# Kernel tuning notes

Measured on AMD Instinct MI355X. Metric: run time of the kernel, lower is better.

Reference implementation:

```python
import jax, jax.numpy as jnp
import numpy as np

D_IN = 512
N_EXPERTS = 32
HID = 16
BATCH = 262144


def setup_inputs() -> dict:
    key = jax.random.key(0)
    kx, kg, k1, kb1, k2, kb2 = jax.random.split(key, 6)
    x = jax.random.normal(kx, (BATCH, D_IN), dtype=jnp.float32)
    # gating: n_experts independent Linear(d_in, 1, bias=False) -> [E, d_in]
    Wg = jax.random.normal(kg, (N_EXPERTS, D_IN), dtype=jnp.float32) * 0.02
    # experts: Linear(d_in,16) -> GELU -> Linear(16,1)
    W1 = jax.random.normal(k1, (N_EXPERTS, D_IN, HID), dtype=jnp.float32) * 0.02
    b1 = jax.random.normal(kb1, (N_EXPERTS, HID), dtype=jnp.float32) * 0.02
    W2 = jax.random.normal(k2, (N_EXPERTS, HID), dtype=jnp.float32) * 0.02
    b2 = jax.random.normal(kb2, (N_EXPERTS,), dtype=jnp.float32) * 0.02
    return {"x": x, "Wg": Wg, "W1": W1, "b1": b1, "W2": W2, "b2": b2}


def reference(x, Wg, W1, b1, W2, b2):
    # gating scores for all experts at once: [B, E]
    gating = jnp.einsum("bd,ed->be", x, Wg)
    gate = jax.nn.softmax(gating, axis=1)  # softmax over experts (torch dim=1)
    # all experts' first layer in one batched GEMM: [B, E, HID]
    h = jax.nn.gelu(jnp.einsum("bd,edh->beh", x, W1) + b1, approximate=False)
    # second layer collapses HID -> scalar per expert: [B, E]
    out = jnp.einsum("beh,eh->be", h, W2) + b2
    # bmm([B,1,E],[B,E,1]) == weighted sum over experts -> [B, 1]
    xi = jnp.sum(out * gate, axis=1, keepdims=True)
    return xi
```

## Files before the change

### kernel.cpp

```cpp
#include <hip/hip_runtime.h>
#include <hip/hip_bf16.h>

#define D_IN 512
#define NEXP 32
#define HID 16
#define NT 34
#define KSTEPS 16
#define BM 128
#define NW 8
#define BATCH 262144

typedef __attribute__((ext_vector_type(8))) short bfrag;
typedef __attribute__((ext_vector_type(4))) float f32x4;

__device__ inline ushort f2bf(float f) {
  uint32_t u = __float_as_uint(f);
  u += 0x7fffu + ((u >> 16) & 1u);
  return (ushort)(u >> 16);
}

__device__ inline bfrag cvt8(const float4 a, const float4 b) {
  union { bfrag v; uint u[4]; } r;
  asm("v_cvt_pk_bf16_f32 %0, %1, %2" : "=v"(r.u[0]) : "v"(a.x), "v"(a.y));
  asm("v_cvt_pk_bf16_f32 %0, %1, %2" : "=v"(r.u[1]) : "v"(a.z), "v"(a.w));
  asm("v_cvt_pk_bf16_f32 %0, %1, %2" : "=v"(r.u[2]) : "v"(b.x), "v"(b.y));
  asm("v_cvt_pk_bf16_f32 %0, %1, %2" : "=v"(r.u[3]) : "v"(b.z), "v"(b.w));
  return r.v;
}

__device__ inline float gelu_t(float v) {
  float t = 0.7978845608028654f * fmaf(0.044715f * v * v, v, v);
  t = fminf(fmaxf(t, -9.f), 9.f);
  float e = __expf(-2.f * t);
  float th = (1.f - e) * __builtin_amdgcn_rcpf(1.f + e);
  return 0.5f * v * (1.f + th);
}

__device__ inline void gload_lds16(const ushort* g, ushort* l) {
  __builtin_amdgcn_global_load_lds(
      (const __attribute__((address_space(1))) void*)g,
      (__attribute__((address_space(3))) void*)l, 16, 0, 0);
}

__global__ void prepack_kernel(const float* __restrict__ Wg,
                               const float* __restrict__ W1,
                               ushort* __restrict__ P) {
  int tid = blockIdx.x * 256 + threadIdx.x;
  const int total = KSTEPS * NT * 64;
  if (tid >= total) return;
  int l  = tid & 63;
  int t  = (tid >> 6) % NT;
  int ks = tid / (NT * 64);
  int n  = t * 16 + (l & 15);
  int kb = ks * 32 + (l >> 4) * 8;
  __align__(16) ushort v[8];
#pragma unroll
  for (int j = 0; j < 8; ++j) {
    int k = kb + j;
    float w;
    if (n < NEXP) {
      w = Wg[n * D_IN + k];
    } else {
      int e = (n - 32) >> 4, h = (n - 32) & 15;
      w = W1[(e * D_IN + k) * HID + h];
    }
    v[j] = f2bf(w);
  }
  *reinterpret_cast<int4*>(P + (size_t)tid * 8) = *reinterpret_cast<const int4*>(v);
}

__global__ __launch_bounds__(512, 2)
void moe_kernel(const float* __restrict__ x, const ushort* __restrict__ P,
                const float* __restrict__ b1, const float* __restrict__ W2,
                const float* __restrict__ b2, float* __restrict__ out) {
  __shared__ __align__(16) ushort Blds[2][NT * 512];
  __shared__ float epi_o[NEXP][BM];
  __shared__ float epi_g[NEXP][BM];
  __shared__ float epi_s[BM];

  const int tid = threadIdx.x;
  const int l = tid & 63;
  const int wid = tid >> 6;
  const int wm = wid >> 1, wn = wid & 1;
  const int lane16 = l & 15, lg = l >> 4;
  const size_t rowBase = (size_t)blockIdx.x * BM;

  f32x4 acc[2][17];
#pragma unroll
  for (int f = 0; f < 2; ++f)
#pragma unroll
    for (int t = 0; t < 17; ++t) acc[f][t] = (f32x4){0.f, 0.f, 0.f, 0.f};

  const float* xp0 = x + (rowBase + wm * 32 + lane16) * D_IN + lg * 8;
  const float* xp1 = xp0 + 16 * D_IN;

  float4 abuf[2][4];

#pragma unroll
  for (int tg = wid; tg < NT; tg += NW)
    gload_lds16(P + ((size_t)tg * 64 + l) * 8, &Blds[0][tg * 512]);
  abuf[0][0] = *reinterpret_cast<const float4*>(xp0);
  abuf[0][1] = *reinterpret_cast<const float4*>(xp0 + 4);
  abuf[0][2] = *reinterpret_cast<const float4*>(xp1);
  abuf[0][3] = *reinterpret_cast<const float4*>(xp1 + 4);
  asm volatile("s_waitcnt vmcnt(4)" ::: "memory");
  __builtin_amdgcn_s_barrier();
  __builtin_amdgcn_sched_barrier(0);

#pragma unroll
  for (int ks = 0; ks < KSTEPS; ++ks) {
    const int cur = ks & 1, nxt = cur ^ 1;
    if (ks < KSTEPS - 1) {
#pragma unroll
      for (int tg = wid; tg < NT; tg += NW)
        gload_lds16(P + ((size_t)((ks + 1) * NT + tg) * 64 + l) * 8,
                    &Blds[nxt][tg * 512]);
      abuf[nxt][0] = *reinterpret_cast<const float4*>(xp0 + (ks + 1) * 32);
      abuf[nxt][1] = *reinterpret_cast<const float4*>(xp0 + (ks + 1) * 32 + 4);
      abuf[nxt][2] = *reinterpret_cast<const float4*>(xp1 + (ks + 1) * 32);
      abuf[nxt][3] = *reinterpret_cast<const float4*>(xp1 + (ks + 1) * 32 + 4);
    }
    const bfrag a0 = cvt8(abuf[cur][0], abuf[cur][1]);
    const bfrag a1 = cvt8(abuf[cur][2], abuf[cur][3]);
#pragma unroll
    for (int t = 0; t < 17; ++t) {
      const bfrag b = *reinterpret_cast<const bfrag*>(&Blds[cur][(wn * 17 + t) * 512 + l * 8]);
      acc[0][t] = __builtin_amdgcn_mfma_f32_16x16x32_bf16(b, a0, acc[0][t], 0, 0, 0);
      acc[1][t] = __builtin_amdgcn_mfma_f32_16x16x32_bf16(b, a1, acc[1][t], 0, 0, 0);
    }
    if (ks < KSTEPS - 1) {
      asm volatile("s_waitcnt vmcnt(4)" ::: "memory");
      __builtin_amdgcn_s_barrier();
      __builtin_amdgcn_sched_barrier(0);
    }
  }

  const int row0 = wm * 32 + lane16;

  if (wn == 0) {
#pragma unroll
    for (int f = 0; f < 2; ++f) {
      const int row = row0 + f * 16;
      float mx = fmaxf(fmaxf(fmaxf(acc[f][0][0], acc[f][0][1]), fmaxf(acc[f][0][2], acc[f][0][3])),
                       fmaxf(fmaxf(acc[f][1][0], acc[f][1][1]), fmaxf(acc[f][1][2], acc[f][1][3])));
      mx = fmaxf(mx, __shfl_xor(mx, 16));
      mx = fmaxf(mx, __shfl_xor(mx, 32));
      float sum = 0.f;
#pragma unroll
      for (int t = 0; t < 2; ++t)
#pragma unroll
        for (int r = 0; r < 4; ++r) {
          float gh = __expf(acc[f][t][r] - mx);
          sum += gh;
          epi_g[t * 16 + lg * 4 + r][row] = gh;
        }
      sum += __shfl_xor(sum, 16);
      sum += __shfl_xor(sum, 32);
      if (lg == 0) epi_s[row] = sum;
    }
#pragma unroll
    for (int t = 2; t < 17; ++t) {
      const int e = t - 2;
      const float4 b1v = *reinterpret_cast<const float4*>(b1 + e * HID + lg * 4);
      const float4 w2v = *reinterpret_cast<const float4*>(W2 + e * HID + lg * 4);
      const float b2v = b2[e];
#pragma unroll
      for (int f = 0; f < 2; ++f) {
        float p = gelu_t(acc[f][t][0] + b1v.x) * w2v.x;
        p = fmaf(gelu_t(acc[f][t][1] + b1v.y), w2v.y, p);
        p = fmaf(gelu_t(acc[f][t][2] + b1v.z), w2v.z, p);
        p = fmaf(gelu_t(acc[f][t][3] + b1v.w), w2v.w, p);
        p += __shfl_xor(p, 16);
        p += __shfl_xor(p, 32);
        if (lg == (t & 3)) epi_o[e][row0 + f * 16] = p + b2v;
      }
    }
  } else {
#pragma unroll
    for (int t = 0; t < 17; ++t) {
      const int e = t + 15;
      const float4 b1v = *reinterpret_cast<const float4*>(b1 + e * HID + lg * 4);
      const float4 w2v = *reinterpret_cast<const float4*>(W2 + e * HID + lg * 4);
      const float b2v = b2[e];
#pragma unroll
      for (int f = 0; f < 2; ++f) {
        float p = gelu_t(acc[f][t][0] + b1v.x) * w2v.x;
        p = fmaf(gelu_t(acc[f][t][1] + b1v.y), w2v.y, p);
        p = fmaf(gelu_t(acc[f][t][2] + b1v.z), w2v.z, p);
        p = fmaf(gelu_t(acc[f][t][3] + b1v.w), w2v.w, p);
        p += __shfl_xor(p, 16);
        p += __shfl_xor(p, 32);
        if (lg == (t & 3)) epi_o[e][row0 + f * 16] = p + b2v;
      }
    }
  }

  __syncthreads();
  if (tid < BM) {
    float a = 0.f;
#pragma unroll
    for (int e = 0; e < NEXP; ++e)
      a = fmaf(epi_o[e][tid], epi_g[e][tid], a);
    out[rowBase + tid] = a / epi_s[tid];
  }
}

extern "C" void kernel_launch(void* const* d_in, const int* in_sizes, int n_in,
                              void* d_out, int out_size, void* d_ws, size_t ws_size,
                              hipStream_t stream) {
  const float* x  = (const float*)d_in[0];
  const float* Wg = (const float*)d_in[1];
  const float* W1 = (const float*)d_in[2];
  const float* b1 = (const float*)d_in[3];
  const float* W2 = (const float*)d_in[4];
  const float* b2 = (const float*)d_in[5];
  float* out = (float*)d_out;
  ushort* P = (ushort*)d_ws;

  hipLaunchKernelGGL(prepack_kernel, dim3((KSTEPS * NT * 64 + 255) / 256), dim3(256),
                     0, stream, Wg, W1, P);
  hipLaunchKernelGGL(moe_kernel, dim3(BATCH / BM), dim3(512),
                     0, stream, x, P, b1, W2, b2, out);
}
```

Measured before the change: 329.6 us.

## Split N tiles across 16 waves and fuse gate-weighted reduction in epilogue

```diff
diff --git a/kernel.cpp b/kernel.cpp
--- a/kernel.cpp
+++ b/kernel.cpp
@@ -7,8 +7,8 @@
 #define NT 34
 #define KSTEPS 16
 #define BM 128
-#define NW 8
 #define BATCH 262144
+#define GXL 129
 
 typedef __attribute__((ext_vector_type(8))) short bfrag;
 typedef __attribute__((ext_vector_type(4))) float f32x4;
@@ -69,40 +69,41 @@
   *reinterpret_cast<int4*>(P + (size_t)tid * 8) = *reinterpret_cast<const int4*>(v);
 }
 
-__global__ __launch_bounds__(512, 2)
+__global__ __launch_bounds__(1024, 4)
 void moe_kernel(const float* __restrict__ x, const ushort* __restrict__ P,
                 const float* __restrict__ b1, const float* __restrict__ W2,
                 const float* __restrict__ b2, float* __restrict__ out) {
   __shared__ __align__(16) ushort Blds[2][NT * 512];
-  __shared__ float epi_o[NEXP][BM];
-  __shared__ float epi_g[NEXP][BM];
-  __shared__ float epi_s[BM];
+  __shared__ float gall[NEXP * GXL];
+  __shared__ float pp[4][BM];
+  __shared__ float sl[BM];
 
   const int tid = threadIdx.x;
   const int l = tid & 63;
   const int wid = tid >> 6;
-  const int wm = wid >> 1, wn = wid & 1;
+  const int wm = wid >> 2, wn = wid & 3;
   const int lane16 = l & 15, lg = l >> 4;
   const size_t rowBase = (size_t)blockIdx.x * BM;
-
-  f32x4 acc[2][17];
+  const int tbase = wn * 8 + (wn > 0);
+
+  f32x4 acc[2][9];
 #pragma unroll
   for (int f = 0; f < 2; ++f)
 #pragma unroll
-    for (int t = 0; t < 17; ++t) acc[f][t] = (f32x4){0.f, 0.f, 0.f, 0.f};
+    for (int t = 0; t < 9; ++t) acc[f][t] = (f32x4){0.f, 0.f, 0.f, 0.f};
 
   const float* xp0 = x + (rowBase + wm * 32 + lane16) * D_IN + lg * 8;
   const float* xp1 = xp0 + 16 * D_IN;
 
-  float4 abuf[2][4];
-
-#pragma unroll
-  for (int tg = wid; tg < NT; tg += NW)
+  float4 abuf[4];
+
+#pragma unroll
+  for (int tg = wid; tg < NT; tg += 16)
     gload_lds16(P + ((size_t)tg * 64 + l) * 8, &Blds[0][tg * 512]);
-  abuf[0][0] = *reinterpret_cast<const float4*>(xp0);
-  abuf[0][1] = *reinterpret_cast<const float4*>(xp0 + 4);
-  abuf[0][2] = *reinterpret_cast<const float4*>(xp1);
-  abuf[0][3] = *reinterpret_cast<const float4*>(xp1 + 4);
+  abuf[0] = *reinterpret_cast<const float4*>(xp0);
+  abuf[1] = *reinterpret_cast<const float4*>(xp0 + 4);
+  abuf[2] = *reinterpret_cast<const float4*>(xp1);
+  abuf[3] = *reinterpret_cast<const float4*>(xp1 + 4);
   asm volatile("s_waitcnt vmcnt(4)" ::: "memory");
   __builtin_amdgcn_s_barrier();
   __builtin_amdgcn_sched_barrier(0);
@@ -110,21 +111,22 @@
 #pragma unroll
   for (int ks = 0; ks < KSTEPS; ++ks) {
     const int cur = ks & 1, nxt = cur ^ 1;
+    const bfrag a0 = cvt8(abuf[0], abuf[1]);
+    const bfrag a1 = cvt8(abuf[2], abuf[3]);
     if (ks < KSTEPS - 1) {
 #pragma unroll
-      for (int tg = wid; tg < NT; tg += NW)
+      for (int tg = wid; tg < NT; tg += 16)
         gload_lds16(P + ((size_t)((ks + 1) * NT + tg) * 64 + l) * 8,
                     &Blds[nxt][tg * 512]);
-      abuf[nxt][0] = *reinterpret_cast<const float4*>(xp0 + (ks + 1) * 32);
-      abuf[nxt][1] = *reinterpret_cast<const float4*>(xp0 + (ks + 1) * 32 + 4);
-      abuf[nxt][2] = *reinterpret_cast<const float4*>(xp1 + (ks + 1) * 32);
-      abuf[nxt][3] = *reinterpret_cast<const float4*>(xp1 + (ks + 1) * 32 + 4);
-    }
-    const bfrag a0 = cvt8(abuf[cur][0], abuf[cur][1]);
-    const bfrag a1 = cvt8(abuf[cur][2], abuf[cur][3]);
-#pragma unroll
-    for (int t = 0; t < 17; ++t) {
-      const bfrag b = *reinterpret_cast<const bfrag*>(&Blds[cur][(wn * 17 + t) * 512 + l * 8]);
+      abuf[0] = *reinterpret_cast<const float4*>(xp0 + (ks + 1) * 32);
+      abuf[1] = *reinterpret_cast<const float4*>(xp0 + (ks + 1) * 32 + 4);
+      abuf[2] = *reinterpret_cast<const float4*>(xp1 + (ks + 1) * 32);
+      abuf[3] = *reinterpret_cast<const float4*>(xp1 + (ks + 1) * 32 + 4);
+    }
+#pragma unroll
+    for (int t = 0; t < 9; ++t) {
+      const bfrag b = *reinterpret_cast<const bfrag*>(
+          &Blds[cur][(tbase + t) * 512 + l * 8]);
       acc[0][t] = __builtin_amdgcn_mfma_f32_16x16x32_bf16(b, a0, acc[0][t], 0, 0, 0);
       acc[1][t] = __builtin_amdgcn_mfma_f32_16x16x32_bf16(b, a1, acc[1][t], 0, 0, 0);
     }
@@ -150,17 +152,24 @@
       for (int t = 0; t < 2; ++t)
 #pragma unroll
         for (int r = 0; r < 4; ++r) {
-          float gh = __expf(acc[f][t][r] - mx);
-          sum += gh;
-          epi_g[t * 16 + lg * 4 + r][row] = gh;
+          float g = __expf(acc[f][t][r] - mx);
+          sum += g;
+          gall[(t * 16 + lg * 4 + r) * GXL + row] = g;
         }
       sum += __shfl_xor(sum, 16);
       sum += __shfl_xor(sum, 32);
-      if (lg == 0) epi_s[row] = sum;
-    }
-#pragma unroll
-    for (int t = 2; t < 17; ++t) {
-      const int e = t - 2;
+      if (lg == 0) sl[row] = sum;
+    }
+  }
+  __syncthreads();
+
+  const int eb = wn * 8 - 1 - (wn == 0);
+  const int tstart = (wn == 0) ? 2 : ((wn == 1) ? 0 : 1);
+  float pacc[2] = {0.f, 0.f};
+#pragma unroll
+  for (int t = 0; t < 9; ++t) {
+    if (t >= tstart) {
+      const int e = eb + t;
       const float4 b1v = *reinterpret_cast<const float4*>(b1 + e * HID + lg * 4);
       const float4 w2v = *reinterpret_cast<const float4*>(W2 + e * HID + lg * 4);
       const float b2v = b2[e];
@@ -172,36 +181,18 @@
         p = fmaf(gelu_t(acc[f][t][3] + b1v.w), w2v.w, p);
         p += __shfl_xor(p, 16);
         p += __shfl_xor(p, 32);
-        if (lg == (t & 3)) epi_o[e][row0 + f * 16] = p + b2v;
+        pacc[f] = fmaf(p + b2v, gall[e * GXL + row0 + f * 16], pacc[f]);
       }
     }
-  } else {
-#pragma unroll
-    for (int t = 0; t < 17; ++t) {
-      const int e = t + 15;
-      const float4 b1v = *reinterpret_cast<const float4*>(b1 + e * HID + lg * 4);
-      const float4 w2v = *reinterpret_cast<const float4*>(W2 + e * HID + lg * 4);
-      const float b2v = b2[e];
-#pragma unroll
-      for (int f = 0; f < 2; ++f) {
-        float p = gelu_t(acc[f][t][0] + b1v.x) * w2v.x;
-        p = fmaf(gelu_t(acc[f][t][1] + b1v.y), w2v.y, p);
-        p = fmaf(gelu_t(acc[f][t][2] + b1v.z), w2v.z, p);
-        p = fmaf(gelu_t(acc[f][t][3] + b1v.w), w2v.w, p);
-        p += __shfl_xor(p, 16);
-        p += __shfl_xor(p, 32);
-        if (lg == (t & 3)) epi_o[e][row0 + f * 16] = p + b2v;
-      }
-    }
-  }
-
+  }
+  if (lg == 0) {
+    pp[wn][row0] = pacc[0];
+    pp[wn][row0 + 16] = pacc[1];
+  }
   __syncthreads();
   if (tid < BM) {
-    float a = 0.f;
-#pragma unroll
-    for (int e = 0; e < NEXP; ++e)
-      a = fmaf(epi_o[e][tid], epi_g[e][tid], a);
-    out[rowBase + tid] = a / epi_s[tid];
+    float a = pp[0][tid] + pp[1][tid] + pp[2][tid] + pp[3][tid];
+    out[rowBase + tid] = a / sl[tid];
   }
 }
 
@@ -219,6 +210,6 @@
 
   hipLaunchKernelGGL(prepack_kernel, dim3((KSTEPS * NT * 64 + 255) / 256), dim3(256),
                      0, stream, Wg, W1, P);
-  hipLaunchKernelGGL(moe_kernel, dim3(BATCH / BM), dim3(512),
+  hipLaunchKernelGGL(moe_kernel, dim3(BATCH / BM), dim3(1024),
                      0, stream, x, P, b1, W2, b2, out);
 }
```

New measurement: 455.7 us. 1.38x slower.
